# Optimization experiments

Hardware: AMD Instinct MI355X
Metric: run time of the kernel (lower is better)

## Reference

```python
import jax, jax.numpy as jnp
import numpy as np

T_OBS, T_PRE, B, IN, E, H = 8, 12, 524288, 2, 16, 8


def setup_inputs() -> dict:
    key = jax.random.key(0)
    ks = jax.random.split(key, 16)
    s = 0.25  # small init scale for weights
    d = {
        "obs_traj_rel": jax.random.normal(ks[0], (T_OBS, B, IN), jnp.float32),
        "pre_traj_rel": jax.random.normal(ks[1], (T_PRE, B, IN), jnp.float32),
        "h0": jax.random.normal(ks[2], (B, H), jnp.float32),
        "c0": jax.random.normal(ks[3], (B, H), jnp.float32),
        "c0_pre": jax.random.normal(ks[4], (B, H), jnp.float32),
        "W_in": jax.random.normal(ks[5], (E, IN), jnp.float32) * s,
        "b_in": jax.random.normal(ks[6], (E,), jnp.float32) * s,
        "W_ih_obs": jax.random.normal(ks[7], (4 * H, E), jnp.float32) * s,
        "W_hh_obs": jax.random.normal(ks[8], (4 * H, H), jnp.float32) * s,
        "b_ih_obs": jax.random.normal(ks[9], (4 * H,), jnp.float32) * s,
        "b_hh_obs": jax.random.normal(ks[10], (4 * H,), jnp.float32) * s,
        "W_ih_pre": jax.random.normal(ks[11], (4 * H, E), jnp.float32) * s,
        "W_hh_pre": jax.random.normal(ks[12], (4 * H, H), jnp.float32) * s,
        "b_ih_pre": jax.random.normal(ks[13], (4 * H,), jnp.float32) * s,
        "b_hh_pre": jax.random.normal(ks[14], (4 * H,), jnp.float32) * s,
    }
    return d


def _lstm_scan(emb, h, c, W_ih, W_hh, b_ih, b_hh):
    """emb: [T, B, E]; PyTorch LSTMCell gate order i, f, g, o."""
    b = b_ih + b_hh

    def step(carry, x):
        h, c = carry
        gates = x @ W_ih.T + h @ W_hh.T + b  # [B, 4H]
        i, f, g, o = jnp.split(gates, 4, axis=-1)
        c = jax.nn.sigmoid(f) * c + jax.nn.sigmoid(i) * jnp.tanh(g)
        h = jax.nn.sigmoid(o) * jnp.tanh(c)
        return (h, c), None

    (h, c), _ = jax.lax.scan(step, (h, c), emb)
    return h, c


def reference(obs_traj_rel, pre_traj_rel, h0, c0, c0_pre,
              W_in, b_in,
              W_ih_obs, W_hh_obs, b_ih_obs, b_hh_obs,
              W_ih_pre, W_hh_pre, b_ih_pre, b_hh_pre):
    batch = obs_traj_rel.shape[1]
    # shared input embedding layer applied to all timesteps at once
    emb_obs = obs_traj_rel @ W_in.T + b_in  # [T_obs, B, E]
    h, c = _lstm_scan(emb_obs, h0, c0, W_ih_obs, W_hh_obs, b_ih_obs, b_hh_obs)
    # faithful to original: permute(1,0).reshape(batch, -1) == transpose then reshape
    c_out = jnp.transpose(h).reshape(batch, -1)
    emb_pre = pre_traj_rel @ W_in.T + b_in  # [T_pre, B, E]
    # hidden_h carries over from obs loop; cell state re-initialized (c0_pre)
    h2, _ = _lstm_scan(emb_pre, h, c0_pre, W_ih_pre, W_hh_pre, b_ih_pre, b_hh_pre)
    x_out = jnp.transpose(h2).reshape(batch, -1)
    return (c_out, x_out)
```

## Files before the change

kernel.cpp:

```cpp
#include <hip/hip_runtime.h>
#include <stdint.h>

#define T_OBS 8
#define T_PRE 12
#define BATCH 524288

#define NLOG2E  (-1.4426950408889634f)
#define P2LOG2E ( 2.8853900817779268f)

typedef __fp16 half8  __attribute__((ext_vector_type(8)));
typedef float  floatx16 __attribute__((ext_vector_type(16)));
typedef unsigned int uint_t;

__device__ __forceinline__ uint_t upk(float a, float b) {
    return __builtin_bit_cast(uint_t, __builtin_amdgcn_cvt_pkrtz(a, b));
}

__global__ void prep_weights(const float* __restrict__ W_in,
                             const float* __restrict__ b_in,
                             const float* __restrict__ W_ih_obs,
                             const float* __restrict__ W_hh_obs,
                             const float* __restrict__ b_ih_obs,
                             const float* __restrict__ b_hh_obs,
                             const float* __restrict__ W_ih_pre,
                             const float* __restrict__ W_hh_pre,
                             const float* __restrict__ b_ih_pre,
                             const float* __restrict__ b_hh_pre,
                             uint_t* __restrict__ wsu) {
    int t = threadIdx.x;
    int phase = t >> 6;
    int l = t & 63;
    int m = l & 31;
    int kh = l >> 5;
    const float* W_ih = phase ? W_ih_pre : W_ih_obs;
    const float* W_hh = phase ? W_hh_pre : W_hh_obs;
    const float* b_ih = phase ? b_ih_pre : b_ih_obs;
    const float* b_hh = phase ? b_hh_pre : b_hh_obs;

    float wx0 = 0.f, wx1 = 0.f;
    float bb = b_ih[m] + b_hh[m];
    #pragma unroll
    for (int e = 0; e < 16; e++) {
        float wie = W_ih[m * 16 + e];
        wx0 += wie * W_in[e * 2 + 0];
        wx1 += wie * W_in[e * 2 + 1];
        bb  += wie * b_in[e];
    }
    float s = (m >= 16 && m < 24) ? P2LOG2E : NLOG2E;

    float af[16];
    af[0] = wx0 * s * 0.5f;
    af[1] = wx1 * s * 0.5f;
    #pragma unroll
    for (int j = 0; j < 4; j++) af[2 + j] = W_hh[m * 8 + j] * s;
    af[6] = bb * s * 0.5f;
    af[7] = 0.f;
    af[8] = af[0];
    af[9] = af[1];
    #pragma unroll
    for (int j = 0; j < 4; j++) af[10 + j] = W_hh[m * 8 + 4 + j] * s;
    af[14] = af[6];
    af[15] = 0.f;

    #pragma unroll
    for (int r = 0; r < 4; r++)
        wsu[phase * 256 + l * 4 + r] = upk(af[kh * 8 + 2 * r], af[kh * 8 + 2 * r + 1]);
}

__device__ __forceinline__ void lstm_step(half8 A, uint_t xpk,
                                          uint_t& pk0, uint_t& pk1,
                                          float c[4], float h[4],
                                          const floatx16& zacc) {
    uint4 bu;
    bu.x = xpk;
    bu.y = pk0;
    bu.z = pk1;
    bu.w = 0x00003C00u;
    half8 B = __builtin_bit_cast(half8, bu);

    floatx16 d = __builtin_amdgcn_mfma_f32_32x32x16_f16(A, B, zacc, 0, 0, 0);

    #pragma unroll
    for (int j = 0; j < 4; j++) {
        float ei = __builtin_amdgcn_exp2f(d[j]);
        float ef = __builtin_amdgcn_exp2f(d[4 + j]);
        float eg = __builtin_amdgcn_exp2f(d[8 + j]);
        float eo = __builtin_amdgcn_exp2f(d[12 + j]);
        float ai  = 1.f + ei;
        float afv = 1.f + ef;
        float ag  = 1.f + eg;
        float gm  = eg - 1.f;
        float p   = ai * ag;
        float num = __builtin_fmaf(c[j], p, gm * afv);
        float cn  = num * __builtin_amdgcn_rcpf(p * afv);
        c[j] = cn;
        float ec = __builtin_amdgcn_exp2f(P2LOG2E * cn);
        h[j] = (ec - 1.f) * __builtin_amdgcn_rcpf((1.f + eo) * (1.f + ec));
    }
    pk0 = upk(h[0], h[1]);
    pk1 = upk(h[2], h[3]);
}

__global__ __launch_bounds__(256, 2)
void lstm_encoder(const float2* __restrict__ obs,
                  const float2* __restrict__ pre,
                  const float4* __restrict__ h0,
                  const float4* __restrict__ c0,
                  const float4* __restrict__ c0p,
                  const uint4* __restrict__ wf,
                  float* __restrict__ out) {
    const int tid  = threadIdx.x;
    const int lane = tid & 63;
    const int wv   = tid >> 6;
    const int n    = lane & 31;
    const int half = lane >> 5;
    const size_t nb = (size_t)blockIdx.x * 128 + wv * 32 + n;

    half8 Aobs = __builtin_bit_cast(half8, wf[lane]);
    half8 Apre = __builtin_bit_cast(half8, wf[64 + lane]);

    floatx16 zacc;
    #pragma unroll
    for (int i = 0; i < 16; i++) zacc[i] = 0.f;

    float4 hv  = h0[nb * 2 + half];
    float4 cv  = c0[nb * 2 + half];
    float4 cv2 = c0p[nb * 2 + half];
    float c[4] = {cv.x, cv.y, cv.z, cv.w};
    float h[4] = {hv.x, hv.y, hv.z, hv.w};
    uint_t pk0 = upk(h[0], h[1]);
    uint_t pk1 = upk(h[2], h[3]);

    float2 xv = obs[nb];
    #pragma unroll 1
    for (int t = 0; t < T_OBS - 1; t++) {
        float2 xn = obs[(size_t)(t + 1) * BATCH + nb];
        lstm_step(Aobs, upk(xv.x, xv.y), pk0, pk1, c, h, zacc);
        xv = xn;
    }
    {
        float2 xn = pre[nb];
        lstm_step(Aobs, upk(xv.x, xv.y), pk0, pk1, c, h, zacc);
        xv = xn;
    }

    #pragma unroll
    for (int j = 0; j < 4; j++)
        out[(size_t)(half * 4 + j) * BATCH + nb] = h[j];

    c[0] = cv2.x; c[1] = cv2.y; c[2] = cv2.z; c[3] = cv2.w;

    #pragma unroll 1
    for (int t = 0; t < T_PRE - 1; t++) {
        float2 xn = pre[(size_t)(t + 1) * BATCH + nb];
        lstm_step(Apre, upk(xv.x, xv.y), pk0, pk1, c, h, zacc);
        xv = xn;
    }
    lstm_step(Apre, upk(xv.x, xv.y), pk0, pk1, c, h, zacc);

    #pragma unroll
    for (int j = 0; j < 4; j++)
        out[(size_t)(8 + half * 4 + j) * BATCH + nb] = h[j];
}

extern "C" void kernel_launch(void* const* d_in, const int* in_sizes, int n_in,
                              void* d_out, int out_size, void* d_ws, size_t ws_size,
                              hipStream_t stream) {
    prep_weights<<<1, 128, 0, stream>>>(
        (const float*)d_in[5],  (const float*)d_in[6],
        (const float*)d_in[7],  (const float*)d_in[8],
        (const float*)d_in[9],  (const float*)d_in[10],
        (const float*)d_in[11], (const float*)d_in[12],
        (const float*)d_in[13], (const float*)d_in[14],
        (uint_t*)d_ws);

    lstm_encoder<<<BATCH / 128, 256, 0, stream>>>(
        (const float2*)d_in[0], (const float2*)d_in[1],
        (const float4*)d_in[2], (const float4*)d_in[3], (const float4*)d_in[4],
        (const uint4*)d_ws, (float*)d_out);
}
```

Before: 218.6 us.

## Process two batch tiles per wave with packed float2 gate activations

```diff
diff --git a/kernel.cpp b/kernel.cpp
--- a/kernel.cpp
+++ b/kernel.cpp
@@ -10,6 +10,7 @@
 
 typedef __fp16 half8  __attribute__((ext_vector_type(8)));
 typedef float  floatx16 __attribute__((ext_vector_type(16)));
+typedef float  f32x2   __attribute__((ext_vector_type(2)));
 typedef unsigned int uint_t;
 
 __device__ __forceinline__ uint_t upk(float a, float b) {
@@ -67,41 +68,71 @@
         wsu[phase * 256 + l * 4 + r] = upk(af[kh * 8 + 2 * r], af[kh * 8 + 2 * r + 1]);
 }
 
-__device__ __forceinline__ void lstm_step(half8 A, uint_t xpk,
-                                          uint_t& pk0, uint_t& pk1,
-                                          float c[4], float h[4],
+__device__ __forceinline__ f32x2 exp2v(f32x2 a) {
+    f32x2 r;
+    r.x = __builtin_amdgcn_exp2f(a.x);
+    r.y = __builtin_amdgcn_exp2f(a.y);
+    return r;
+}
+__device__ __forceinline__ f32x2 rcpv(f32x2 a) {
+    f32x2 r;
+    r.x = __builtin_amdgcn_rcpf(a.x);
+    r.y = __builtin_amdgcn_rcpf(a.y);
+    return r;
+}
+
+__device__ __forceinline__ void act_pair(f32x2 gi, f32x2 gf, f32x2 gg, f32x2 go,
+                                         f32x2& c, f32x2& h) {
+    f32x2 ei = exp2v(gi);
+    f32x2 ef = exp2v(gf);
+    f32x2 eg = exp2v(gg);
+    f32x2 eo = exp2v(go);
+    f32x2 ai = ei + 1.f;
+    f32x2 af = ef + 1.f;
+    f32x2 ag = eg + 1.f;
+    f32x2 gm = eg - 1.f;
+    f32x2 p  = ai * ag;
+    f32x2 num = c * p + gm * af;
+    f32x2 cn  = num * rcpv(p * af);
+    c = cn;
+    f32x2 ec = exp2v(P2LOG2E * cn);
+    h = (ec - 1.f) * rcpv((eo + 1.f) * (ec + 1.f));
+}
+
+struct Tile {
+    f32x2 c01, c23;
+    f32x2 h01, h23;
+    uint_t pk0, pk1;
+};
+
+__device__ __forceinline__ void lstm_step(half8 A, uint_t xpk, Tile& T,
                                           const floatx16& zacc) {
     uint4 bu;
     bu.x = xpk;
-    bu.y = pk0;
-    bu.z = pk1;
+    bu.y = T.pk0;
+    bu.z = T.pk1;
     bu.w = 0x00003C00u;
     half8 B = __builtin_bit_cast(half8, bu);
 
     floatx16 d = __builtin_amdgcn_mfma_f32_32x32x16_f16(A, B, zacc, 0, 0, 0);
 
-    #pragma unroll
-    for (int j = 0; j < 4; j++) {
-        float ei = __builtin_amdgcn_exp2f(d[j]);
-        float ef = __builtin_amdgcn_exp2f(d[4 + j]);
-        float eg = __builtin_amdgcn_exp2f(d[8 + j]);
-        float eo = __builtin_amdgcn_exp2f(d[12 + j]);
-        float ai  = 1.f + ei;
-        float afv = 1.f + ef;
-        float ag  = 1.f + eg;
-        float gm  = eg - 1.f;
-        float p   = ai * ag;
-        float num = __builtin_fmaf(c[j], p, gm * afv);
-        float cn  = num * __builtin_amdgcn_rcpf(p * afv);
-        c[j] = cn;
-        float ec = __builtin_amdgcn_exp2f(P2LOG2E * cn);
-        h[j] = (ec - 1.f) * __builtin_amdgcn_rcpf((1.f + eo) * (1.f + ec));
-    }
-    pk0 = upk(h[0], h[1]);
-    pk1 = upk(h[2], h[3]);
-}
-
-__global__ __launch_bounds__(256, 2)
+    f32x2 gi, gf, gg, go;
+    gi.x = d[0];  gi.y = d[1];
+    gf.x = d[4];  gf.y = d[5];
+    gg.x = d[8];  gg.y = d[9];
+    go.x = d[12]; go.y = d[13];
+    act_pair(gi, gf, gg, go, T.c01, T.h01);
+    gi.x = d[2];  gi.y = d[3];
+    gf.x = d[6];  gf.y = d[7];
+    gg.x = d[10]; gg.y = d[11];
+    go.x = d[14]; go.y = d[15];
+    act_pair(gi, gf, gg, go, T.c23, T.h23);
+
+    T.pk0 = upk(T.h01.x, T.h01.y);
+    T.pk1 = upk(T.h23.x, T.h23.y);
+}
+
+__global__ __launch_bounds__(256, 4)
 void lstm_encoder(const float2* __restrict__ obs,
                   const float2* __restrict__ pre,
                   const float4* __restrict__ h0,
@@ -114,7 +145,8 @@
     const int wv   = tid >> 6;
     const int n    = lane & 31;
     const int half = lane >> 5;
-    const size_t nb = (size_t)blockIdx.x * 128 + wv * 32 + n;
+    const size_t nbA = (size_t)blockIdx.x * 256 + wv * 64 + n;
+    const size_t nbB = nbA + 32;
 
     half8 Aobs = __builtin_bit_cast(half8, wf[lane]);
     half8 Apre = __builtin_bit_cast(half8, wf[64 + lane]);
@@ -123,44 +155,69 @@
     #pragma unroll
     for (int i = 0; i < 16; i++) zacc[i] = 0.f;
 
-    float4 hv  = h0[nb * 2 + half];
-    float4 cv  = c0[nb * 2 + half];
-    float4 cv2 = c0p[nb * 2 + half];
-    float c[4] = {cv.x, cv.y, cv.z, cv.w};
-    float h[4] = {hv.x, hv.y, hv.z, hv.w};
-    uint_t pk0 = upk(h[0], h[1]);
-    uint_t pk1 = upk(h[2], h[3]);
-
-    float2 xv = obs[nb];
+    Tile TA, TB;
+    {
+        float4 hvA = h0[nbA * 2 + half];
+        float4 cvA = c0[nbA * 2 + half];
+        float4 hvB = h0[nbB * 2 + half];
+        float4 cvB = c0[nbB * 2 + half];
+        TA.c01.x = cvA.x; TA.c01.y = cvA.y; TA.c23.x = cvA.z; TA.c23.y = cvA.w;
+        TB.c01.x = cvB.x; TB.c01.y = cvB.y; TB.c23.x = cvB.z; TB.c23.y = cvB.w;
+        TA.pk0 = upk(hvA.x, hvA.y); TA.pk1 = upk(hvA.z, hvA.w);
+        TB.pk0 = upk(hvB.x, hvB.y); TB.pk1 = upk(hvB.z, hvB.w);
+    }
+    float4 cvA2 = c0p[nbA * 2 + half];
+    float4 cvB2 = c0p[nbB * 2 + half];
+
+    float2 xvA = obs[nbA];
+    float2 xvB = obs[nbB];
     #pragma unroll 1
     for (int t = 0; t < T_OBS - 1; t++) {
-        float2 xn = obs[(size_t)(t + 1) * BATCH + nb];
-        lstm_step(Aobs, upk(xv.x, xv.y), pk0, pk1, c, h, zacc);
-        xv = xn;
+        float2 xnA = obs[(size_t)(t + 1) * BATCH + nbA];
+        float2 xnB = obs[(size_t)(t + 1) * BATCH + nbB];
+        lstm_step(Aobs, upk(xvA.x, xvA.y), TA, zacc);
+        lstm_step(Aobs, upk(xvB.x, xvB.y), TB, zacc);
+        xvA = xnA; xvB = xnB;
     }
     {
-        float2 xn = pre[nb];
-        lstm_step(Aobs, upk(xv.x, xv.y), pk0, pk1, c, h, zacc);
-        xv = xn;
-    }
-
-    #pragma unroll
-    for (int j = 0; j < 4; j++)
-        out[(size_t)(half * 4 + j) * BATCH + nb] = h[j];
-
-    c[0] = cv2.x; c[1] = cv2.y; c[2] = cv2.z; c[3] = cv2.w;
+        float2 xnA = pre[nbA];
+        float2 xnB = pre[nbB];
+        lstm_step(Aobs, upk(xvA.x, xvA.y), TA, zacc);
+        lstm_step(Aobs, upk(xvB.x, xvB.y), TB, zacc);
+        xvA = xnA; xvB = xnB;
+    }
+
+    out[(size_t)(half * 4 + 0) * BATCH + nbA] = TA.h01.x;
+    out[(size_t)(half * 4 + 1) * BATCH + nbA] = TA.h01.y;
+    out[(size_t)(half * 4 + 2) * BATCH + nbA] = TA.h23.x;
+    out[(size_t)(half * 4 + 3) * BATCH + nbA] = TA.h23.y;
+    out[(size_t)(half * 4 + 0) * BATCH + nbB] = TB.h01.x;
+    out[(size_t)(half * 4 + 1) * BATCH + nbB] = TB.h01.y;
+    out[(size_t)(half * 4 + 2) * BATCH + nbB] = TB.h23.x;
+    out[(size_t)(half * 4 + 3) * BATCH + nbB] = TB.h23.y;
+
+    TA.c01.x = cvA2.x; TA.c01.y = cvA2.y; TA.c23.x = cvA2.z; TA.c23.y = cvA2.w;
+    TB.c01.x = cvB2.x; TB.c01.y = cvB2.y; TB.c23.x = cvB2.z; TB.c23.y = cvB2.w;
 
     #pragma unroll 1
     for (int t = 0; t < T_PRE - 1; t++) {
-        float2 xn = pre[(size_t)(t + 1) * BATCH + nb];
-        lstm_step(Apre, upk(xv.x, xv.y), pk0, pk1, c, h, zacc);
-        xv = xn;
-    }
-    lstm_step(Apre, upk(xv.x, xv.y), pk0, pk1, c, h, zacc);
-
-    #pragma unroll
-    for (int j = 0; j < 4; j++)
-        out[(size_t)(8 + half * 4 + j) * BATCH + nb] = h[j];
+        float2 xnA = pre[(size_t)(t + 1) * BATCH + nbA];
+        float2 xnB = pre[(size_t)(t + 1) * BATCH + nbB];
+        lstm_step(Apre, upk(xvA.x, xvA.y), TA, zacc);
+        lstm_step(Apre, upk(xvB.x, xvB.y), TB, zacc);
+        xvA = xnA; xvB = xnB;
+    }
+    lstm_step(Apre, upk(xvA.x, xvA.y), TA, zacc);
+    lstm_step(Apre, upk(xvB.x, xvB.y), TB, zacc);
+
+    out[(size_t)(8 + half * 4 + 0) * BATCH + nbA] = TA.h01.x;
+    out[(size_t)(8 + half * 4 + 1) * BATCH + nbA] = TA.h01.y;
+    out[(size_t)(8 + half * 4 + 2) * BATCH + nbA] = TA.h23.x;
+    out[(size_t)(8 + half * 4 + 3) * BATCH + nbA] = TA.h23.y;
+    out[(size_t)(8 + half * 4 + 0) * BATCH + nbB] = TB.h01.x;
+    out[(size_t)(8 + half * 4 + 1) * BATCH + nbB] = TB.h01.y;
+    out[(size_t)(8 + half * 4 + 2) * BATCH + nbB] = TB.h23.x;
+    out[(size_t)(8 + half * 4 + 3) * BATCH + nbB] = TB.h23.y;
 }
 
 extern "C" void kernel_launch(void* const* d_in, const int* in_sizes, int n_in,
@@ -174,7 +231,7 @@
         (const float*)d_in[13], (const float*)d_in[14],
         (uint_t*)d_ws);
 
-    lstm_encoder<<<BATCH / 128, 256, 0, stream>>>(
+    lstm_encoder<<<BATCH / 256, 256, 0, stream>>>(
         (const float2*)d_in[0], (const float2*)d_in[1],
         (const float4*)d_in[2], (const float4*)d_in[3], (const float4*)d_in[4],
         (const uint4*)d_ws, (float*)d_out);
```

New measurement: 212.0 us. 1.03x faster.
